# Performance work log

Measured on AMD Instinct MI355X. Metric: run time of the kernel, lower is better.

Reference implementation:

```python
import jax, jax.numpy as jnp
import numpy as np

B, S, D, H, NH = 128, 512, 64, 256, 8
HD = H // NH
NEG = -10000000000.0


def _ln(x, g, b, eps=1e-5):
    m = x.mean(-1, keepdims=True)
    v = ((x - m) ** 2).mean(-1, keepdims=True)
    return (x - m) * jax.lax.rsqrt(v + eps) * g + b


def _mha(xq, xkv, mask, qW, qb, kW, kb, vW, vb, oW, ob):
    # mask: [B,1,1,S_kv] bool, True = masked out
    b, sq, _ = xq.shape
    sk = xkv.shape[1]
    Q = (xq @ qW + qb).reshape(b, sq, NH, HD).transpose(0, 2, 1, 3)
    K = (xkv @ kW + kb).reshape(b, sk, NH, HD).transpose(0, 2, 1, 3)
    V = (xkv @ vW + vb).reshape(b, sk, NH, HD).transpose(0, 2, 1, 3)
    energy = jnp.einsum('bhqd,bhkd->bhqk', Q, K) / jnp.sqrt(jnp.float32(HD))
    energy = jnp.where(mask, NEG, energy)
    attn = jax.nn.softmax(energy, axis=-1)  # dropout is identity in eval
    x = jnp.einsum('bhqk,bhkd->bhqd', attn, V)
    x = x.transpose(0, 2, 1, 3).reshape(b, sq, H)
    return x @ oW + ob


def _ffn(x, f1W, f1b, f2W, f2b):
    # NewGELU == tanh-approximate GELU (GPT-2)
    return jax.nn.gelu(x @ f1W + f1b, approximate=True) @ f2W + f2b


def _fwd(src, ln0sg, ln0sb, ln0tg, ln0tb, semW, semb, temW, temb,
         e_qW, e_qb, e_kW, e_kb, e_vW, e_vb, e_oW, e_ob, e_ln1g, e_ln1b,
         e_f1W, e_f1b, e_f2W, e_f2b, e_ln2g, e_ln2b,
         d_sqW, d_sqb, d_skW, d_skb, d_svW, d_svb, d_soW, d_sob, d_ln1g, d_ln1b,
         d_eqW, d_eqb, d_ekW, d_ekb, d_evW, d_evb, d_eoW, d_eob, d_ln2g, d_ln2b,
         d_f1W, d_f1b, d_f2W, d_f2b, d_ln3g, d_ln3b, outW, outb):
    valid = src.sum(-1) != 0                      # [B,S] (prod_fea == 0)
    amask = (~valid)[:, None, None, :]            # [B,1,1,S]; trg==src so trg_mask==src_mask
    embs_src = _ln(src, ln0sg, ln0sb) @ semW + semb   # emb_need
    embs_trg = _ln(src, ln0tg, ln0tb) @ temW + temb
    # encoder layer
    a = _mha(embs_src, embs_src, amask, e_qW, e_qb, e_kW, e_kb, e_vW, e_vb, e_oW, e_ob)
    x = _ln(embs_src + a, e_ln1g, e_ln1b)
    enc_src = _ln(x + _ffn(x, e_f1W, e_f1b, e_f2W, e_f2b), e_ln2g, e_ln2b)
    # decoder layer
    a = _mha(embs_trg, embs_trg, amask, d_sqW, d_sqb, d_skW, d_skb, d_svW, d_svb, d_soW, d_sob)
    t = _ln(embs_trg + a, d_ln1g, d_ln1b)
    a = _mha(t, enc_src, amask, d_eqW, d_eqb, d_ekW, d_ekb, d_evW, d_evb, d_eoW, d_eob)
    t = _ln(t + a, d_ln2g, d_ln2b)
    t = _ln(t + _ffn(t, d_f1W, d_f1b, d_f2W, d_f2b), d_ln3g, d_ln3b)
    logits = (t @ outW + outb)[..., 0]            # [B,S]
    p = jnp.exp(logits) * valid.astype(logits.dtype)
    return p / p.sum(-1, keepdims=True)           # multi_purchase=False branch


def setup_inputs() -> dict:
    key = jax.random.key(0)
    keys = iter(jax.random.split(key, 64))
    inp = {"src": jax.random.normal(next(keys), (B, S, D), dtype=jnp.float32)}

    def lin(name, i, o):
        inp[name + "W"] = jax.random.normal(next(keys), (i, o), dtype=jnp.float32) * 0.02
        inp[name + "b"] = jnp.zeros((o,), dtype=jnp.float32)

    def ln(name, d):
        inp[name + "g"] = jnp.ones((d,), dtype=jnp.float32)
        inp[name + "b"] = jnp.zeros((d,), dtype=jnp.float32)

    ln("ln0s", D); ln("ln0t", D)
    lin("sem", D, H); lin("tem", D, H)
    for n in ["e_q", "e_k", "e_v", "e_o"]:
        lin(n, H, H)
    ln("e_ln1", H); lin("e_f1", H, H); lin("e_f2", H, H); ln("e_ln2", H)
    for n in ["d_sq", "d_sk", "d_sv", "d_so", "d_eq", "d_ek", "d_ev", "d_eo"]:
        lin(n, H, H)
    ln("d_ln1", H); ln("d_ln2", H)
    lin("d_f1", H, H); lin("d_f2", H, H); ln("d_ln3", H)
    lin("out", H, 1)
    return inp


def reference(src, ln0sg, ln0sb, ln0tg, ln0tb, semW, semb, temW, temb,
              e_qW, e_qb, e_kW, e_kb, e_vW, e_vb, e_oW, e_ob, e_ln1g, e_ln1b,
              e_f1W, e_f1b, e_f2W, e_f2b, e_ln2g, e_ln2b,
              d_sqW, d_sqb, d_skW, d_skb, d_svW, d_svb, d_soW, d_sob, d_ln1g, d_ln1b,
              d_eqW, d_eqb, d_ekW, d_ekb, d_evW, d_evb, d_eoW, d_eob, d_ln2g, d_ln2b,
              d_f1W, d_f1b, d_f2W, d_f2b, d_ln3g, d_ln3b, outW, outb):
    return _fwd(src, ln0sg, ln0sb, ln0tg, ln0tb, semW, semb, temW, temb,
                e_qW, e_qb, e_kW, e_kb, e_vW, e_vb, e_oW, e_ob, e_ln1g, e_ln1b,
                e_f1W, e_f1b, e_f2W, e_f2b, e_ln2g, e_ln2b,
                d_sqW, d_sqb, d_skW, d_skb, d_svW, d_svb, d_soW, d_sob, d_ln1g, d_ln1b,
                d_eqW, d_eqb, d_ekW, d_ekb, d_evW, d_evb, d_eoW, d_eob, d_ln2g, d_ln2b,
                d_f1W, d_f1b, d_f2W, d_f2b, d_ln3g, d_ln3b, outW, outb)
```

## Files before the change

kernel.cpp:

```cpp
#include <hip/hip_runtime.h>
#include <hip/hip_bf16.h>


#define Bb  128
#define Ss  512
#define Hh  256
#define NHh 8
#define Mm  (Bb*Ss)

typedef unsigned short bf16_t;
typedef __attribute__((ext_vector_type(8))) short short8;
typedef __attribute__((ext_vector_type(4))) float f32x4;

__device__ __forceinline__ float bf2f(bf16_t h){
  union { unsigned int u; float f; } v; v.u = ((unsigned int)h)<<16; return v.f;
}
__device__ __forceinline__ bf16_t f2bf(float f){
  union { float f; unsigned int u; } v; v.f = f;
  unsigned int r = (v.u + 0x7fffu + ((v.u>>16)&1u)) >> 16;
  return (bf16_t)r;
}
__device__ __forceinline__ unsigned pk_bf16(float a, float b){
  union { __hip_bfloat162 h; unsigned u; } v;
  v.h = __float22bfloat162_rn(float2{a,b});
  return v.u;
}
__device__ __forceinline__ short8 ld_bf8(const bf16_t* p){
  union { uint4 u; short8 s; } v; v.u = *(const uint4*)p; return v.s;
}
__device__ __forceinline__ void gload16(const bf16_t* g, bf16_t* l){
  __builtin_amdgcn_global_load_lds(
      (const __attribute__((address_space(1))) void*)g,
      (__attribute__((address_space(3))) void*)l, 16, 0, 0);
}
__device__ __forceinline__ float exp2_hw(float x){
  float r; asm("v_exp_f32 %0, %1" : "=v"(r) : "v"(x)); return r;
}
__device__ __forceinline__ float gelu_f(float x){
  float u = 0.7978845608028654f*(x + 0.044715f*x*x*x);
  float e = __expf(2.0f*u);
  float th = 1.0f - 2.0f*__builtin_amdgcn_rcpf(e + 1.0f);
  return 0.5f*x*(1.0f + th);
}

struct PrepDesc { const float* s; unsigned off; int K; };
struct Prep18  { PrepDesc d[18]; };

__global__ __launch_bounds__(256) void k_prep(Prep18 p, bf16_t* __restrict__ arena)
{
  PrepDesc dd = p.d[blockIdx.y];
  int i = blockIdx.x*256 + threadIdx.x;
  if (i < dd.K*256){
    int k = i>>8, n = i&255;
    arena[dd.off + n*dd.K + k] = f2bf(dd.s[i]);
  }
}

__global__ __launch_bounds__(256) void k_ln0(const float* __restrict__ src,
    const float* __restrict__ gs, const float* __restrict__ bs,
    const float* __restrict__ gt, const float* __restrict__ bt,
    bf16_t* __restrict__ xs, bf16_t* __restrict__ xt, float* __restrict__ valid)
{
  int row  = blockIdx.x*4 + (threadIdx.x>>6);
  int lane = threadIdx.x & 63;
  float x = src[(size_t)row*64 + lane];
  float s = x;
  #pragma unroll
  for (int o=32;o>0;o>>=1) s += __shfl_xor(s,o);
  float mean = s*(1.0f/64.0f);
  float d = x - mean;
  float ss = d*d;
  #pragma unroll
  for (int o=32;o>0;o>>=1) ss += __shfl_xor(ss,o);
  float r = rsqrtf(ss*(1.0f/64.0f) + 1e-5f);
  float xn = d*r;
  xs[(size_t)row*64+lane] = f2bf(xn*gs[lane] + bs[lane]);
  xt[(size_t)row*64+lane] = f2bf(xn*gt[lane] + bt[lane]);
  if (lane==0) valid[row] = (s != 0.0f) ? 1.0f : 0.0f;
}

template<int EPI, int OUTM, int KK>
__global__ __launch_bounds__(512,2) void k_wgemm(const bf16_t* __restrict__ A,
    const bf16_t* __restrict__ Wt, const float* __restrict__ bias,
    void* __restrict__ Cv, const bf16_t* __restrict__ Pres,
    const float* __restrict__ g, const float* __restrict__ bb,
    const float* __restrict__ oW, const float* __restrict__ obp, float cs)
{
  constexpr int NKC  = KK/32;
  constexpr int IDS  = 16*NKC;
  constexpr int PERW = IDS/8;
  __shared__ bf16_t Ws[IDS*512];

  int t = threadIdx.x, w = t>>6, lane = t&63, l15 = lane&15, quad = lane>>4;
  int r0 = blockIdx.x*256 + w*32;

  #pragma unroll
  for (int j=0; j<PERW; j++){
    int id = w*PERW + j; int kc = id>>4, nt = id&15;
    gload16(Wt + (size_t)(nt*16 + l15)*KK + kc*32 + quad*8, &Ws[id*512]);
  }
  short8 a0 = ld_bf8(A + (size_t)(r0      + l15)*KK + quad*8);
  short8 a1 = ld_bf8(A + (size_t)(r0 + 16 + l15)*KK + quad*8);
  __syncthreads();

  f32x4 z = {0.f,0.f,0.f,0.f};
  f32x4 acc0[16], acc1[16];
  #pragma unroll
  for (int nt=0; nt<16; nt++){ acc0[nt] = z; acc1[nt] = z; }

  #pragma unroll
  for (int kc=0; kc<NKC; kc++){
    short8 a0n, a1n;
    if (kc+1 < NKC){
      a0n = ld_bf8(A + (size_t)(r0      + l15)*KK + (kc+1)*32 + quad*8);
      a1n = ld_bf8(A + (size_t)(r0 + 16 + l15)*KK + (kc+1)*32 + quad*8);
    }
    #pragma unroll
    for (int nt=0; nt<16; nt++){
      short8 b = ld_bf8(&Ws[(kc*16 + nt)*512 + lane*8]);
      acc0[nt] = __builtin_amdgcn_mfma_f32_16x16x32_bf16(a0, b, acc0[nt], 0,0,0);
      acc1[nt] = __builtin_amdgcn_mfma_f32_16x16x32_bf16(a1, b, acc1[nt], 0,0,0);
    }
    a0 = a0n; a1 = a1n;
  }

  float bv[16];
  #pragma unroll
  for (int nt=0; nt<16; nt++) bv[nt] = bias[nt*16 + l15];

  if (OUTM==0){
    auto epi = [&](f32x4 (&ac)[16], int tt){
      int rowb = r0 + tt*16 + quad*4;
      #pragma unroll
      for (int nt=0; nt<16; nt++)
        #pragma unroll
        for (int r=0; r<4; r++){
          float v = ac[nt][r] + bv[nt];
          v = (EPI==1) ? gelu_f(v) : v*cs;
          ((bf16_t*)Cv)[(size_t)(rowb + r)*256 + nt*16 + l15] = f2bf(v);
        }
    };
    epi(acc0, 0); epi(acc1, 1);
  } else if (OUTM==2){
    auto epi = [&](f32x4 (&ac)[16], int tt){
      int m = r0 + tt*16 + quad*4;
      #pragma unroll
      for (int nt=0; nt<16; nt++){
        int col = nt*16 + l15;
        uint2 pk = { pk_bf16(ac[nt][0]+bv[nt], ac[nt][1]+bv[nt]),
                     pk_bf16(ac[nt][2]+bv[nt], ac[nt][3]+bv[nt]) };
        *(uint2*)&((bf16_t*)Cv)[((size_t)((m>>9)*256 + col))*512 + (m&511)] = pk;
      }
    };
    epi(acc0, 0); epi(acc1, 1);
  } else {
    float gv[16], bbv[16], wv[16];
    #pragma unroll
    for (int nt=0; nt<16; nt++){ gv[nt] = g[nt*16+l15]; bbv[nt] = bb[nt*16+l15]; }
    if (OUTM==5)
      #pragma unroll
      for (int nt=0; nt<16; nt++) wv[nt] = oW[nt*16+l15];
    float ob0 = (OUTM==5) ? obp[0] : 0.f;

    auto epi = [&](f32x4 (&ac)[16], int tt){
      #pragma unroll
      for (int r=0; r<4; r++){
        int row = r0 + tt*16 + quad*4 + r;
        const bf16_t* pr = Pres + (size_t)row*256;
        float v[16]; float s = 0.f, q = 0.f;
        #pragma unroll
        for (int nt=0; nt<16; nt++){
          v[nt] = ac[nt][r] + bv[nt] + bf2f(pr[nt*16 + l15]);
          s += v[nt]; q += v[nt]*v[nt];
        }
        s += __shfl_xor(s,1); s += __shfl_xor(s,2);
        s += __shfl_xor(s,4); s += __shfl_xor(s,8);
        q += __shfl_xor(q,1); q += __shfl_xor(q,2);
        q += __shfl_xor(q,4); q += __shfl_xor(q,8);
        float mean = s*(1.0f/256.0f);
        float var  = q*(1.0f/256.0f) - mean*mean;
        float rstd = rsqrtf(var + 1e-5f);
        if (OUTM==3){
          bf16_t* po = (bf16_t*)Cv + (size_t)row*256;
          #pragma unroll
          for (int nt=0; nt<16; nt++)
            po[nt*16 + l15] = f2bf((v[nt]-mean)*rstd*gv[nt] + bbv[nt]);
        } else {
          float s2 = 0.f;
          #pragma unroll
          for (int nt=0; nt<16; nt++)
            s2 += ((v[nt]-mean)*rstd*gv[nt] + bbv[nt]) * wv[nt];
          s2 += __shfl_xor(s2,1); s2 += __shfl_xor(s2,2);
          s2 += __shfl_xor(s2,4); s2 += __shfl_xor(s2,8);
          if (l15==0) ((float*)Cv)[row] = s2 + ob0;
        }
      }
    };
    epi(acc0, 0); epi(acc1, 1);
  }
}

__global__ __launch_bounds__(256) void k_attn(const bf16_t* __restrict__ Qm,
    const bf16_t* __restrict__ Km, const bf16_t* __restrict__ VT,
    const float* __restrict__ valid, bf16_t* __restrict__ AO)
{
  __shared__ bf16_t Pbuf[4][2][2][16][40];
  __shared__ float  Smask[512];
  int t = threadIdx.x, wave = t>>6, lane = t&63, l15 = lane&15, quad = lane>>4;
  int lid = blockIdx.x + 8*blockIdx.y + 1024*blockIdx.z;
  int hp = lid & 3, pb = (lid>>2)&1, g = (lid>>3)&7, bh = lid>>6;
  int h  = hp*2 + (g&1);
  int qc = g>>1;
  int b  = bh*2 + pb;
  int q0 = qc*128;

  Smask[t]     = (valid[b*Ss + t      ] != 0.f) ? 0.f : -1.44269504e10f;
  Smask[t+256] = (valid[b*Ss + t + 256] != 0.f) ? 0.f : -1.44269504e10f;
  __syncthreads();

  short8 aQ0 = ld_bf8(Qm + (size_t)(b*Ss + q0 + (wave*2  )*16 + l15)*256 + h*32 + quad*8);
  short8 aQ1 = ld_bf8(Qm + (size_t)(b*Ss + q0 + (wave*2+1)*16 + l15)*256 + h*32 + quad*8);
  const bf16_t* Kb = Km + (size_t)(b*Ss)*256 + h*32;
  const bf16_t* Vb = VT + ((size_t)b*256 + h*32)*512;

  f32x4 z = {0.f,0.f,0.f,0.f};
  f32x4 O0[2] = {z,z}, O1[2] = {z,z};
  float ls0 = 0.f, ls1 = 0.f;

  auto process = [&](int kt2n, short8 K0, short8 K1){
    int s = kt2n & 1;
    #pragma unroll
    for (int half=0; half<2; half++){
      short8 aK = half ? K1 : K0;
      int ktile = kt2n*2 + half;
      __builtin_amdgcn_s_setprio(1);
      f32x4 s0 = __builtin_amdgcn_mfma_f32_16x16x32_bf16(aK, aQ0, z, 0,0,0);
      f32x4 s1 = __builtin_amdgcn_mfma_f32_16x16x32_bf16(aK, aQ1, z, 0,0,0);
      __builtin_amdgcn_s_setprio(0);
      float4 mb = *(const float4*)&Smask[ktile*16 + quad*4];
      float p00 = exp2_hw(s0[0] + mb.x);
      float p01 = exp2_hw(s0[1] + mb.y);
      float p02 = exp2_hw(s0[2] + mb.z);
      float p03 = exp2_hw(s0[3] + mb.w);
      float p10 = exp2_hw(s1[0] + mb.x);
      float p11 = exp2_hw(s1[1] + mb.y);
      float p12 = exp2_hw(s1[2] + mb.z);
      float p13 = exp2_hw(s1[3] + mb.w);
      ls0 += (p00+p01)+(p02+p03);
      ls1 += (p10+p11)+(p12+p13);
      uint2 w0 = { pk_bf16(p00,p01), pk_bf16(p02,p03) };
      uint2 w1 = { pk_bf16(p10,p11), pk_bf16(p12,p13) };
      *(uint2*)&Pbuf[wave][0][s][l15][half*16 + quad*4] = w0;
      *(uint2*)&Pbuf[wave][1][s][l15][half*16 + quad*4] = w1;
    }
  };
  auto loadK = [&](int n, short8& K0, short8& K1){
    K0 = ld_bf8(Kb + (size_t)((n*2  )*16 + l15)*256 + quad*8);
    K1 = ld_bf8(Kb + (size_t)((n*2+1)*16 + l15)*256 + quad*8);
  };
  auto loadV = [&](int n, short8& V0, short8& V1){
    V0 = ld_bf8(Vb + (size_t)(l15   )*512 + n*32 + quad*8);
    V1 = ld_bf8(Vb + (size_t)(16+l15)*512 + n*32 + quad*8);
  };

  short8 cK0, cK1, pK0, pK1, nK0, nK1;
  short8 cV0, cV1, mV0, mV1, nV0, nV1;
  loadK(0, cK0, cK1);
  process(0, cK0, cK1);
  loadK(1, pK0, pK1);
  loadV(0, cV0, cV1);
  loadV(1, mV0, mV1);

  #pragma unroll 2
  for (int kt2=0; kt2<16; kt2++){
    if (kt2+2 < 16){ loadK(kt2+2, nK0, nK1); loadV(kt2+2, nV0, nV1); }
    int s = kt2 & 1;
    short8 aP0 = ld_bf8(&Pbuf[wave][0][s][l15][quad*8]);
    short8 aP1 = ld_bf8(&Pbuf[wave][1][s][l15][quad*8]);
    __builtin_amdgcn_s_setprio(1);
    O0[0] = __builtin_amdgcn_mfma_f32_16x16x32_bf16(aP0, cV0, O0[0], 0,0,0);
    O0[1] = __builtin_amdgcn_mfma_f32_16x16x32_bf16(aP0, cV1, O0[1], 0,0,0);
    O1[0] = __builtin_amdgcn_mfma_f32_16x16x32_bf16(aP1, cV0, O1[0], 0,0,0);
    O1[1] = __builtin_amdgcn_mfma_f32_16x16x32_bf16(aP1, cV1, O1[1], 0,0,0);
    __builtin_amdgcn_s_setprio(0);
    if (kt2+1 < 16) process(kt2+1, pK0, pK1);
    pK0 = nK0; pK1 = nK1;
    cV0 = mV0; cV1 = mV1; mV0 = nV0; mV1 = nV1;
  }

  ls0 += __shfl_xor(ls0,16); ls0 += __shfl_xor(ls0,32);
  ls1 += __shfl_xor(ls1,16); ls1 += __shfl_xor(ls1,32);
  float linv0 = (ls0 > 0.f) ? 1.0f/ls0 : 0.f;
  float linv1 = (ls1 > 0.f) ? 1.0f/ls1 : 0.f;
  float i0[4], i1[4];
  #pragma unroll
  for (int r=0; r<4; r++){
    i0[r] = __shfl(linv0, quad*4 + r);
    i1[r] = __shfl(linv1, quad*4 + r);
  }
  size_t r0 = (size_t)(b*Ss + q0 + (wave*2  )*16);
  size_t r1 = (size_t)(b*Ss + q0 + (wave*2+1)*16);
  #pragma unroll
  for (int nt=0; nt<2; nt++)
    #pragma unroll
    for (int r=0; r<4; r++){
      AO[(r0 + quad*4 + r)*256 + h*32 + nt*16 + l15] = f2bf(O0[nt][r]*i0[r]);
      AO[(r1 + quad*4 + r)*256 + h*32 + nt*16 + l15] = f2bf(O1[nt][r]*i1[r]);
    }
}

__global__ __launch_bounds__(256) void k_final(const float* __restrict__ L,
    const float* __restrict__ valid, float* __restrict__ out)
{
  __shared__ float wsum[4];
  int b = blockIdx.x, t = threadIdx.x;
  float e0 = __expf(L[b*Ss + t      ]) * valid[b*Ss + t      ];
  float e1 = __expf(L[b*Ss + 256 + t]) * valid[b*Ss + 256 + t];
  float s = e0 + e1;
  #pragma unroll
  for (int o=32;o>0;o>>=1) s += __shfl_xor(s,o);
  if ((t&63)==0) wsum[t>>6] = s;
  __syncthreads();
  float tot = wsum[0]+wsum[1]+wsum[2]+wsum[3];
  out[b*Ss + t      ] = e0/tot;
  out[b*Ss + 256 + t] = e1/tot;
}

extern "C" void kernel_launch(void* const* d_in, const int* in_sizes, int n_in,
                              void* d_out, int out_size, void* d_ws, size_t ws_size,
                              hipStream_t stream)
{
  #define F(i) ((const float*)d_in[(i)])
  bool sig = (in_sizes[33] == 256);
  const float* d_eqW  = F(sig?35:33); const float* d_eqb  = F(sig?36:34);
  const float* d_ekW  = F(sig?37:35); const float* d_ekb  = F(sig?38:36);
  const float* d_evW  = F(sig?39:37); const float* d_evb  = F(sig?40:38);
  const float* d_eoW  = F(sig?41:39); const float* d_eob  = F(sig?42:40);
  const float* d_ln1g = F(sig?33:41); const float* d_ln1b = F(sig?34:42);

  char* w = (char*)d_ws;
  bf16_t* P0 = (bf16_t*)w; w += (size_t)Mm*Hh*2;
  bf16_t* P1 = (bf16_t*)w; w += (size_t)Mm*Hh*2;
  bf16_t* H0 = (bf16_t*)w; w += (size_t)Mm*Hh*2;
  bf16_t* H1 = (bf16_t*)w;
  bf16_t* xs = (bf16_t*)w; w += (size_t)Mm*Hh*2;
  bf16_t* H2 = (bf16_t*)w;
  bf16_t* xt = (bf16_t*)w; w += (size_t)Mm*Hh*2;
  bf16_t* Wa = (bf16_t*)w; w += (size_t)(2*16384 + 16*65536)*2;
  float*  valid  = (float*)w; w += (size_t)Mm*4;
  float*  logits = (float*)w; w += (size_t)Mm*4;
  float* out = (float*)d_out;

  unsigned o_sem = 0, o_tem = 16384;
  unsigned o_w[16]; for (int i=0;i<16;i++) o_w[i] = 32768 + i*65536u;
  Prep18 pp;
  const float* srcs[18] = { F(5), F(7), F(9), F(11), F(13), F(15), F(19), F(21),
                            F(25), F(27), F(29), F(31), d_eqW, d_ekW, d_evW, d_eoW,
                            F(45), F(47) };
  unsigned offs[18] = { o_sem, o_tem, o_w[0],o_w[1],o_w[2],o_w[3],o_w[4],o_w[5],
                        o_w[6],o_w[7],o_w[8],o_w[9],o_w[10],o_w[11],o_w[12],o_w[13],
                        o_w[14],o_w[15] };
  for (int i=0;i<18;i++){ pp.d[i].s = srcs[i]; pp.d[i].off = offs[i]; pp.d[i].K = (i<2)?64:256; }

  dim3 blk(256);
  dim3 blk512(512);
  dim3 gLN(Mm/4);
  dim3 gW(256);
  dim3 gA(NHh, Bb, 4);
  dim3 gP(256, 18);
  const float* NF = nullptr; const bf16_t* NB = nullptr;
  const float QS = 0.17677669529663687f * 1.4426950408889634f;

  k_prep<<<gP, blk, 0, stream>>>(pp, Wa);
  k_ln0<<<gLN, blk, 0, stream>>>(F(0), F(1),F(2), F(3),F(4), xs, xt, valid);

  k_wgemm<0,0,64><<<gW, blk512, 0, stream>>>(xs, Wa+o_sem, F(6), P0, NB, NF,NF,NF,NF, 1.0f);
  k_wgemm<0,0,64><<<gW, blk512, 0, stream>>>(xt, Wa+o_tem, F(8), P1, NB, NF,NF,NF,NF, 1.0f);

  k_wgemm<0,0,256><<<gW, blk512, 0, stream>>>(P0, Wa+o_w[0], F(10), H0, NB, NF,NF,NF,NF, QS);
  k_wgemm<0,0,256><<<gW, blk512, 0, stream>>>(P0, Wa+o_w[1], F(12), H1, NB, NF,NF,NF,NF, 1.0f);
  k_wgemm<0,2,256><<<gW, blk512, 0, stream>>>(P0, Wa+o_w[2], F(14), H2, NB, NF,NF,NF,NF, 1.0f);
  k_attn<<<gA, blk, 0, stream>>>(H0, H1, H2, valid, H0);
  k_wgemm<0,3,256><<<gW, blk512, 0, stream>>>(H0, Wa+o_w[3], F(16), P0, P0, F(17),F(18), NF,NF, 1.0f);
  k_wgemm<1,0,256><<<gW, blk512, 0, stream>>>(P0, Wa+o_w[4], F(20), H0, NB, NF,NF,NF,NF, 1.0f);
  k_wgemm<0,3,256><<<gW, blk512, 0, stream>>>(H0, Wa+o_w[5], F(22), P0, P0, F(23),F(24), NF,NF, 1.0f);

  k_wgemm<0,0,256><<<gW, blk512, 0, stream>>>(P1, Wa+o_w[6], F(26), H0, NB, NF,NF,NF,NF, QS);
  k_wgemm<0,0,256><<<gW, blk512, 0, stream>>>(P1, Wa+o_w[7], F(28), H1, NB, NF,NF,NF,NF, 1.0f);
  k_wgemm<0,2,256><<<gW, blk512, 0, stream>>>(P1, Wa+o_w[8], F(30), H2, NB, NF,NF,NF,NF, 1.0f);
  k_attn<<<gA, blk, 0, stream>>>(H0, H1, H2, valid, H0);
  k_wgemm<0,3,256><<<gW, blk512, 0, stream>>>(H0, Wa+o_w[9], F(32), P1, P1, d_ln1g,d_ln1b, NF,NF, 1.0f);

  k_wgemm<0,0,256><<<gW, blk512, 0, stream>>>(P1, Wa+o_w[10], d_eqb, H0, NB, NF,NF,NF,NF, QS);
  k_wgemm<0,0,256><<<gW, blk512, 0, stream>>>(P0, Wa+o_w[11], d_ekb, H1, NB, NF,NF,NF,NF, 1.0f);
  k_wgemm<0,2,256><<<gW, blk512, 0, stream>>>(P0, Wa+o_w[12], d_evb, H2, NB, NF,NF,NF,NF, 1.0f);
  k_attn<<<gA, blk, 0, stream>>>(H0, H1, H2, valid, H0);
  k_wgemm<0,3,256><<<gW, blk512, 0, stream>>>(H0, Wa+o_w[13], d_eob, P1, P1, F(43),F(44), NF,NF, 1.0f);

  k_wgemm<1,0,256><<<gW, blk512, 0, stream>>>(P1, Wa+o_w[14], F(46), H0, NB, NF,NF,NF,NF, 1.0f);
  k_wgemm<0,5,256><<<gW, blk512, 0, stream>>>(H0, Wa+o_w[15], F(48), logits, P1, F(49),F(50), F(51),F(52), 1.0f);

  k_final<<<dim3(Bb), blk, 0, stream>>>(logits, valid, out);
  #undef F
}
```

Baseline: 929.2 us.

## Give each attention wave four query tiles to reuse K/V loads

Each wave in the attention kernel now handles four 16-row query tiles instead of two, so each block covers 256 queries and the grid's z dimension is halved. Every K and V fragment loaded from global memory now feeds twice as many MFMAs, which cuts redundant K/V traffic per query. The P staging buffer loses its double-buffer slot, and the change raises register pressure while halving the block count. With a single P slot there is a possible hazard between the P writes in process and the P reads in the next iteration, though the order within one wave is sequential.

```diff
diff --git a/kernel.cpp b/kernel.cpp
--- a/kernel.cpp
+++ b/kernel.cpp
@@ -204,54 +204,52 @@
     const bf16_t* __restrict__ Km, const bf16_t* __restrict__ VT,
     const float* __restrict__ valid, bf16_t* __restrict__ AO)
 {
-  __shared__ bf16_t Pbuf[4][2][2][16][40];
+  __shared__ bf16_t Pbuf[4][4][16][40];
   __shared__ float  Smask[512];
   int t = threadIdx.x, wave = t>>6, lane = t&63, l15 = lane&15, quad = lane>>4;
   int lid = blockIdx.x + 8*blockIdx.y + 1024*blockIdx.z;
-  int hp = lid & 3, pb = (lid>>2)&1, g = (lid>>3)&7, bh = lid>>6;
+  int hp = lid & 3, pb = (lid>>2)&1, g = (lid>>3)&3, bh = lid>>5;
   int h  = hp*2 + (g&1);
   int qc = g>>1;
   int b  = bh*2 + pb;
-  int q0 = qc*128;
+  int q0 = qc*256 + wave*64;
 
   Smask[t]     = (valid[b*Ss + t      ] != 0.f) ? 0.f : -1.44269504e10f;
   Smask[t+256] = (valid[b*Ss + t + 256] != 0.f) ? 0.f : -1.44269504e10f;
   __syncthreads();
 
-  short8 aQ0 = ld_bf8(Qm + (size_t)(b*Ss + q0 + (wave*2  )*16 + l15)*256 + h*32 + quad*8);
-  short8 aQ1 = ld_bf8(Qm + (size_t)(b*Ss + q0 + (wave*2+1)*16 + l15)*256 + h*32 + quad*8);
+  short8 aQ[4];
+  #pragma unroll
+  for (int qt=0; qt<4; qt++)
+    aQ[qt] = ld_bf8(Qm + (size_t)(b*Ss + q0 + qt*16 + l15)*256 + h*32 + quad*8);
   const bf16_t* Kb = Km + (size_t)(b*Ss)*256 + h*32;
   const bf16_t* Vb = VT + ((size_t)b*256 + h*32)*512;
 
   f32x4 z = {0.f,0.f,0.f,0.f};
-  f32x4 O0[2] = {z,z}, O1[2] = {z,z};
-  float ls0 = 0.f, ls1 = 0.f;
+  f32x4 O[4][2];
+  #pragma unroll
+  for (int qt=0; qt<4; qt++){ O[qt][0] = z; O[qt][1] = z; }
+  float ls[4] = {0.f,0.f,0.f,0.f};
 
   auto process = [&](int kt2n, short8 K0, short8 K1){
-    int s = kt2n & 1;
     #pragma unroll
     for (int half=0; half<2; half++){
       short8 aK = half ? K1 : K0;
       int ktile = kt2n*2 + half;
-      __builtin_amdgcn_s_setprio(1);
-      f32x4 s0 = __builtin_amdgcn_mfma_f32_16x16x32_bf16(aK, aQ0, z, 0,0,0);
-      f32x4 s1 = __builtin_amdgcn_mfma_f32_16x16x32_bf16(aK, aQ1, z, 0,0,0);
-      __builtin_amdgcn_s_setprio(0);
       float4 mb = *(const float4*)&Smask[ktile*16 + quad*4];
-      float p00 = exp2_hw(s0[0] + mb.x);
-      float p01 = exp2_hw(s0[1] + mb.y);
-      float p02 = exp2_hw(s0[2] + mb.z);
-      float p03 = exp2_hw(s0[3] + mb.w);
-      float p10 = exp2_hw(s1[0] + mb.x);
-      float p11 = exp2_hw(s1[1] + mb.y);
-      float p12 = exp2_hw(s1[2] + mb.z);
-      float p13 = exp2_hw(s1[3] + mb.w);
-      ls0 += (p00+p01)+(p02+p03);
-      ls1 += (p10+p11)+(p12+p13);
-      uint2 w0 = { pk_bf16(p00,p01), pk_bf16(p02,p03) };
-      uint2 w1 = { pk_bf16(p10,p11), pk_bf16(p12,p13) };
-      *(uint2*)&Pbuf[wave][0][s][l15][half*16 + quad*4] = w0;
-      *(uint2*)&Pbuf[wave][1][s][l15][half*16 + quad*4] = w1;
+      #pragma unroll
+      for (int qt=0; qt<4; qt++){
+        __builtin_amdgcn_s_setprio(1);
+        f32x4 sq = __builtin_amdgcn_mfma_f32_16x16x32_bf16(aK, aQ[qt], z, 0,0,0);
+        __builtin_amdgcn_s_setprio(0);
+        float p0 = exp2_hw(sq[0] + mb.x);
+        float p1 = exp2_hw(sq[1] + mb.y);
+        float p2 = exp2_hw(sq[2] + mb.z);
+        float p3 = exp2_hw(sq[3] + mb.w);
+        ls[qt] += (p0+p1)+(p2+p3);
+        uint2 wq = { pk_bf16(p0,p1), pk_bf16(p2,p3) };
+        *(uint2*)&Pbuf[wave][qt][l15][half*16 + quad*4] = wq;
+      }
     }
   };
   auto loadK = [&](int n, short8& K0, short8& K1){
@@ -274,39 +272,37 @@
   #pragma unroll 2
   for (int kt2=0; kt2<16; kt2++){
     if (kt2+2 < 16){ loadK(kt2+2, nK0, nK1); loadV(kt2+2, nV0, nV1); }
-    int s = kt2 & 1;
-    short8 aP0 = ld_bf8(&Pbuf[wave][0][s][l15][quad*8]);
-    short8 aP1 = ld_bf8(&Pbuf[wave][1][s][l15][quad*8]);
+    short8 aP[4];
+    #pragma unroll
+    for (int qt=0; qt<4; qt++)
+      aP[qt] = ld_bf8(&Pbuf[wave][qt][l15][quad*8]);
     __builtin_amdgcn_s_setprio(1);
-    O0[0] = __builtin_amdgcn_mfma_f32_16x16x32_bf16(aP0, cV0, O0[0], 0,0,0);
-    O0[1] = __builtin_amdgcn_mfma_f32_16x16x32_bf16(aP0, cV1, O0[1], 0,0,0);
-    O1[0] = __builtin_amdgcn_mfma_f32_16x16x32_bf16(aP1, cV0, O1[0], 0,0,0);
-    O1[1] = __builtin_amdgcn_mfma_f32_16x16x32_bf16(aP1, cV1, O1[1], 0,0,0);
+    #pragma unroll
+    for (int qt=0; qt<4; qt++){
+      O[qt][0] = __builtin_amdgcn_mfma_f32_16x16x32_bf16(aP[qt], cV0, O[qt][0], 0,0,0);
+      O[qt][1] = __builtin_amdgcn_mfma_f32_16x16x32_bf16(aP[qt], cV1, O[qt][1], 0,0,0);
+    }
     __builtin_amdgcn_s_setprio(0);
     if (kt2+1 < 16) process(kt2+1, pK0, pK1);
     pK0 = nK0; pK1 = nK1;
     cV0 = mV0; cV1 = mV1; mV0 = nV0; mV1 = nV1;
   }
 
-  ls0 += __shfl_xor(ls0,16); ls0 += __shfl_xor(ls0,32);
-  ls1 += __shfl_xor(ls1,16); ls1 += __shfl_xor(ls1,32);
-  float linv0 = (ls0 > 0.f) ? 1.0f/ls0 : 0.f;
-  float linv1 = (ls1 > 0.f) ? 1.0f/ls1 : 0.f;
-  float i0[4], i1[4];
-  #pragma unroll
-  for (int r=0; r<4; r++){
-    i0[r] = __shfl(linv0, quad*4 + r);
-    i1[r] = __shfl(linv1, quad*4 + r);
-  }
-  size_t r0 = (size_t)(b*Ss + q0 + (wave*2  )*16);
-  size_t r1 = (size_t)(b*Ss + q0 + (wave*2+1)*16);
-  #pragma unroll
-  for (int nt=0; nt<2; nt++)
-    #pragma unroll
-    for (int r=0; r<4; r++){
-      AO[(r0 + quad*4 + r)*256 + h*32 + nt*16 + l15] = f2bf(O0[nt][r]*i0[r]);
-      AO[(r1 + quad*4 + r)*256 + h*32 + nt*16 + l15] = f2bf(O1[nt][r]*i1[r]);
-    }
+  #pragma unroll
+  for (int qt=0; qt<4; qt++){
+    float l = ls[qt];
+    l += __shfl_xor(l,16); l += __shfl_xor(l,32);
+    float linv = (l > 0.f) ? 1.0f/l : 0.f;
+    float iv[4];
+    #pragma unroll
+    for (int r=0; r<4; r++) iv[r] = __shfl(linv, quad*4 + r);
+    size_t rq = (size_t)(b*Ss + q0 + qt*16);
+    #pragma unroll
+    for (int nt=0; nt<2; nt++)
+      #pragma unroll
+      for (int r=0; r<4; r++)
+        AO[(rq + quad*4 + r)*256 + h*32 + nt*16 + l15] = f2bf(O[qt][nt][r]*iv[r]);
+  }
 }
 
 __global__ __launch_bounds__(256) void k_final(const float* __restrict__ L,
@@ -366,7 +362,7 @@
   dim3 blk512(512);
   dim3 gLN(Mm/4);
   dim3 gW(256);
-  dim3 gA(NHh, Bb, 4);
+  dim3 gA(NHh, Bb, 2);
   dim3 gP(256, 18);
   const float* NF = nullptr; const bf16_t* NB = nullptr;
   const float QS = 0.17677669529663687f * 1.4426950408889634f;
```

Result: no change. 926.6 us (-0.3%).
